# Kernel optimization log

Hardware: AMD Instinct MI355X
Metric: run time of the kernel (lower is better)

Reference implementation:

```python
import jax, jax.numpy as jnp
import numpy as np

# ---- problem sizes (would come from edge_index / init args in the torch module) ----
N = 10000      # number of nodes
E = 100000     # number of edges
C = 6          # channels per node
L = 6          # layers
B = 16         # batch
N_IN = 100     # input nodes  (nodes [0, N_IN))
N_OUT = 100    # output nodes (nodes [N-N_OUT, N))
EPS = 1e-5


def setup_inputs() -> dict:
    rng = np.random.default_rng(0)
    src = rng.integers(0, N, size=E).astype(np.int32)
    dst = rng.integers(0, N, size=E).astype(np.int32)

    input_mask = np.zeros(N, bool); input_mask[:N_IN] = True
    output_mask = np.zeros(N, bool); output_mask[N - N_OUT:] = True
    func_mask = ~(input_mask | output_mask)
    func_nodes = np.nonzero(func_mask)[0].astype(np.int32)
    F = func_nodes.size
    ii = np.arange(C, dtype=np.int32)

    # W1 (E -> C*N): edge e feeds all C channels of its dst node. nnz = E*C
    w1_rows = np.repeat(np.arange(E, dtype=np.int32), C)
    w1_cols = (dst[:, None] * C + ii[None, :]).reshape(-1)

    # W2 (C*N -> C*N): dense CxC block per function node. nnz = F*C*C
    base = np.repeat(func_nodes * C, C * C)
    w2_rows = base + np.tile(np.repeat(ii, C), F)
    w2_cols = base + np.tile(np.tile(ii, C), F)

    # W3 (C*N -> E): edge e reads the C channels of src(e) if src is a function node
    e_sel = np.nonzero(func_mask[src])[0].astype(np.int32)
    w3_rows = (src[e_sel][:, None] * C + ii[None, :]).reshape(-1)
    w3_cols = np.repeat(e_sel, C)

    # values: kaiming-style init with fan d (d=C for W1/W2, d=1 for W3)
    w1_vals = (rng.standard_normal(w1_rows.size) / np.sqrt(C)).astype(np.float32)
    w2_vals = (rng.standard_normal(w2_rows.size) / np.sqrt(C)).astype(np.float32)
    w3_vals = (rng.standard_normal(w3_rows.size) * 1.0).astype(np.float32)

    key = jax.random.key(0)
    x = jax.random.normal(key, (B, N), dtype=jnp.float32)

    return {
        "x": x,
        "src": jnp.asarray(src), "dst": jnp.asarray(dst),
        "output_mask": jnp.asarray(output_mask),
        "w1_rows": jnp.asarray(w1_rows), "w1_cols": jnp.asarray(w1_cols),
        "w1_vals": jnp.asarray(w1_vals), "b1": jnp.zeros((C * N,), jnp.float32),
        "w2_rows": jnp.asarray(w2_rows), "w2_cols": jnp.asarray(w2_cols),
        "w2_vals": jnp.asarray(w2_vals), "b2": jnp.zeros((C * N,), jnp.float32),
        "w3_rows": jnp.asarray(w3_rows), "w3_cols": jnp.asarray(w3_cols),
        "w3_vals": jnp.asarray(w3_vals), "b3": jnp.zeros((E,), jnp.float32),
        "gamma": jnp.ones((L,), jnp.float32), "beta": jnp.zeros((L,), jnp.float32),
    }


def _sp_lin(h, rows, cols, vals, bias, out_dim):
    # out[b, c] = sum_{k: cols[k]==c} h[b, rows[k]] * vals[k] + bias[c]
    contrib = h[:, rows] * vals  # [B, nnz]
    out = jnp.zeros((h.shape[0], out_dim), h.dtype).at[:, cols].add(contrib)
    return out + bias


def _batchnorm_scalar(z, g, b):
    # BatchNorm1d(1) on z.view(-1,1): single channel over all B*E elements (training mode)
    m = jnp.mean(z)
    v = jnp.mean(jnp.square(z - m))
    return (z - m) * jax.lax.rsqrt(v + EPS) * g + b


def reference(x, src, dst, output_mask,
              w1_rows, w1_cols, w1_vals, b1,
              w2_rows, w2_cols, w2_vals, b2,
              w3_rows, w3_cols, w3_vals, b3,
              gamma, beta):
    x0 = x[:, src]          # node2edge: [B, E]
    h = x0
    h_last = x0             # residual=True path
    for l in range(L):
        z = _sp_lin(h, w1_rows, w1_cols, w1_vals, b1, C * N)
        z = jax.nn.elu(z)
        z = _sp_lin(z, w2_rows, w2_cols, w2_vals, b2, C * N)
        z = jax.nn.elu(z)
        z = _sp_lin(z, w3_rows, w3_cols, w3_vals, b3, E)
        z = _batchnorm_scalar(z, gamma[l], beta[l])
        h = z + h_last
        h_last = h
    h = h / L
    # edge2node: scatter edge values to dst nodes, keep only output nodes
    node = jnp.zeros((x.shape[0], N), x.dtype).at[:, dst].add(h)
    return jnp.where(output_mask[None, :], node, 0.0)
```

## Files before the change

kernel.cpp:

```cpp
#include <hip/hip_runtime.h>
#include <math.h>

#define NN 10000
#define NE 100000
#define CC 6
#define LL 6
#define BB 16
#define FUNC_LO 100
#define FUNC_HI 9900
#define NOUT 100
#define EPSF 1e-5f
#define NSLOT 64

struct Slot { double s1, s2; double pad[6]; };

struct Params {
  const float *x, *w1v, *b1, *w2v, *b2, *w3v, *b3, *gamma, *beta;
  const int *src, *dst, *w3r, *w3c;
  float *out;
  int *row_start, *counts, *fill, *slot;
  int *row2, *counts2, *fill2, *csr2;
  uint4 *grec;
  uint4 *srec;
  unsigned short *sb3;
  float *xT, *h;
  unsigned short *z3a, *z3b;
  unsigned short *A;
  float *Cw;
  Slot *part, *baseS;
  int F, Ksel;
};

__device__ __forceinline__ float eluf(float x){ return x > 0.0f ? x : expm1f(x); }
__device__ __forceinline__ float bf2f(unsigned short h){
  union { unsigned int u; float f; } c; c.u = ((unsigned int)h)<<16; return c.f;
}
__device__ __forceinline__ unsigned short f2bf(float f){
  union { float f; unsigned int u; } c; c.f = f;
  return (unsigned short)((c.u + 0x7FFFu + ((c.u>>16)&1u)) >> 16);
}
__device__ __forceinline__ unsigned int packbf(float a, float b){
  return (unsigned int)f2bf(a) | ((unsigned int)f2bf(b)<<16);
}
__device__ __forceinline__ float2 ubf2(unsigned int u){
  union { unsigned int u; float f; } lo, hi;
  lo.u = u<<16; hi.u = u & 0xFFFF0000u;
  return make_float2(lo.f, hi.f);
}

__device__ void block_add_slot(double a, double q, Slot* sl){
  __shared__ double sb1[4], sb2[4];
  #pragma unroll
  for(int off=32;off;off>>=1){ a+=__shfl_down(a,off); q+=__shfl_down(q,off); }
  int wid = threadIdx.x>>6;
  if((threadIdx.x&63)==0){ sb1[wid]=a; sb2[wid]=q; }
  __syncthreads();
  if(threadIdx.x==0){
    double A=sb1[0]+sb1[1]+sb1[2]+sb1[3];
    double Q=sb2[0]+sb2[1]+sb2[2]+sb2[3];
    if(A!=0.0) atomicAdd(&sl->s1,A);
    if(Q!=0.0) atomicAdd(&sl->s2,Q);
  }
  __syncthreads();
}

__device__ void bn_params(const Slot* part, const Slot* baseS, float* m, float* inv){
  __shared__ double s_mv[2];
  if(threadIdx.x < NSLOT){
    double a = part[threadIdx.x].s1 + baseS[threadIdx.x].s1;
    double q = part[threadIdx.x].s2 + baseS[threadIdx.x].s2;
    #pragma unroll
    for(int off=32;off;off>>=1){ a+=__shfl_down(a,off); q+=__shfl_down(q,off); }
    if(threadIdx.x==0){
      const double cnt = (double)NE*(double)BB;
      double md = a/cnt, vd = q/cnt - md*md;
      s_mv[0]=md; s_mv[1]=1.0/sqrt(vd+(double)EPSF);
    }
  }
  __syncthreads();
  *m=(float)s_mv[0]; *inv=(float)s_mv[1];
  __syncthreads();
}

__global__ __launch_bounds__(256) void kw_P1(Params p){
  int tid = blockIdx.x*256 + threadIdx.x, nt = gridDim.x*256;
  for(int i=tid;i<NN*BB;i+=nt){ int n=i>>4, b=i&15; p.xT[i]=p.x[b*NN+n]; }
  for(int i=tid;i<BB*NN;i+=nt) p.out[i]=0.f;
  double a=0.0,q=0.0;
  for(int e=tid;e<NE;e+=nt){
    atomicAdd(&p.counts[p.dst[e]],1);
    int s=p.src[e];
    if(!(s>=FUNC_LO && s<FUNC_HI)){ double v=(double)p.b3[e]; a+=v; q+=v*v; }
  }
  for(int k=tid;k<p.Ksel;k+=nt){
    int s=p.w3r[k*CC]/CC;
    atomicAdd(&p.counts2[s-FUNC_LO],1);
  }
  block_add_slot(a*BB, q*BB, &p.baseS[blockIdx.x&(NSLOT-1)]);
}

__global__ __launch_bounds__(256) void kw_scan(Params p){
  __shared__ int s_scan[256];
  const int*  cin  = (blockIdx.x==0)? p.counts : p.counts2;
  int*        rout = (blockIdx.x==0)? p.row_start : p.row2;
  const int   nel  = (blockIdx.x==0)? NN : p.F;
  const int   CH   = (nel+255)/256;
  int t=threadIdx.x, base=t*CH, s=0;
  for(int k=0;k<CH;k++){ int i=base+k; if(i<nel) s+=cin[i]; }
  s_scan[t]=s; __syncthreads();
  for(int off=1;off<256;off<<=1){
    int v=(t>=off)?s_scan[t-off]:0; __syncthreads();
    s_scan[t]+=v; __syncthreads();
  }
  int run=s_scan[t]-s;
  for(int k=0;k<CH;k++){ int i=base+k; if(i<nel){ rout[i]=run; run+=cin[i]; } }
  if(t==255) rout[nel]=s_scan[255];
}

__global__ __launch_bounds__(256) void kw_fill(Params p){
  int tid = blockIdx.x*256 + threadIdx.x, nt = gridDim.x*256;
  for(int e=tid;e<NE;e+=nt){
    int n=p.dst[e];
    int pos=p.row_start[n]+atomicAdd(&p.fill[n],1);
    p.slot[e]=pos;
    const float* w=&p.w1v[e*CC];
    int s=p.src[e];
    float b3v=p.b3[e];
    p.grec[pos]=make_uint4(packbf(w[0],w[1]),packbf(w[2],w[3]),
                           packbf(w[4],w[5]),(unsigned int)s);
    if(!(s>=FUNC_LO && s<FUNC_HI)){
      unsigned int hb = f2bf(b3v);
      unsigned int pk = hb | (hb<<16);
      uint4 v4 = make_uint4(pk,pk,pk,pk);
      uint4* za=(uint4*)&p.z3a[pos*BB];
      uint4* zb=(uint4*)&p.z3b[pos*BB];
      za[0]=v4; za[1]=v4; zb[0]=v4; zb[1]=v4;
    }
  }
  for(int k=tid;k<p.Ksel;k+=nt){
    int fi=p.w3r[k*CC]/CC - FUNC_LO;
    int pos=p.row2[fi]+atomicAdd(&p.fill2[fi],1);
    p.csr2[pos]=k;
  }
}

template<int MODE>
__global__ __launch_bounds__(256) void kw_AB(Params p, int l,
    const unsigned short* __restrict__ z3p, unsigned short* __restrict__ z3c){
  int tid = blockIdx.x*256 + (int)threadIdx.x, nt = gridDim.x*256;
  float c1=0.f, c2=0.f;
  if(MODE>0){
    float m, inv;
    bn_params(p.part+(l-1)*NSLOT, p.baseS, &m, &inv);
    float g=p.gamma[l-1], be=p.beta[l-1];
    c1 = inv*g; c2 = be - m*c1;
  }
  const int FB2 = p.F*32;
  double a=0.0, q=0.0;
  for(int t=tid;t<FB2;t+=nt){
    int fi = t>>5;
    int u  = t&31, b = u&15, half = u>>4;
    int n  = FUNC_LO+fi;
    float acc[CC], cacc[CC];
    #pragma unroll
    for(int i=0;i<CC;i++){ acc[i]=0.f; cacc[i]=0.f; }
    int beg=p.row_start[n], end=p.row_start[n+1];
    int pp = beg + half;
    for(; pp+2<end; pp+=4){
      uint4 g0=p.grec[pp], g1=p.grec[pp+2];
      float2 wa0=ubf2(g0.x), wb0=ubf2(g0.y), wc0=ubf2(g0.z);
      float2 wa1=ubf2(g1.x), wb1=ubf2(g1.y), wc1=ubf2(g1.z);
      float hv0, hv1;
      if(MODE==0){
        int s0=(int)g0.w, s1=(int)g1.w;
        hv0 = p.xT[s0*BB+b];
        hv1 = p.xT[s1*BB+b];
        cacc[0]+=wa0.x+wa1.x; cacc[1]+=wa0.y+wa1.y; cacc[2]+=wb0.x+wb1.x;
        cacc[3]+=wb0.y+wb1.y; cacc[4]+=wc0.x+wc1.x; cacc[5]+=wc0.y+wc1.y;
      } else {
        hv0 = bf2f(z3p[pp*BB+b]);
        hv1 = bf2f(z3p[(pp+2)*BB+b]);
      }
      acc[0]+=hv0*wa0.x+hv1*wa1.x; acc[1]+=hv0*wa0.y+hv1*wa1.y;
      acc[2]+=hv0*wb0.x+hv1*wb1.x; acc[3]+=hv0*wb0.y+hv1*wb1.y;
      acc[4]+=hv0*wc0.x+hv1*wc1.x; acc[5]+=hv0*wc0.y+hv1*wc1.y;
    }
    if(pp<end){
      uint4 g0=p.grec[pp];
      float2 wa0=ubf2(g0.x), wb0=ubf2(g0.y), wc0=ubf2(g0.z);
      float hv0;
      if(MODE==0){
        int s0=(int)g0.w;
        hv0 = p.xT[s0*BB+b];
        cacc[0]+=wa0.x; cacc[1]+=wa0.y; cacc[2]+=wb0.x;
        cacc[3]+=wb0.y; cacc[4]+=wc0.x; cacc[5]+=wc0.y;
      } else {
        hv0 = bf2f(z3p[pp*BB+b]);
      }
      acc[0]+=hv0*wa0.x; acc[1]+=hv0*wa0.y; acc[2]+=hv0*wb0.x;
      acc[3]+=hv0*wb0.y; acc[4]+=hv0*wc0.x; acc[5]+=hv0*wc0.y;
    }
    float z1v[CC];
    #pragma unroll
    for(int i=0;i<CC;i++){
      acc[i] += __shfl_xor(acc[i],16);
      if(MODE==0){
        cacc[i] += __shfl_xor(cacc[i],16);
        if(half==0){
          p.A[(fi*CC+i)*BB+b] = f2bf(acc[i]);
          if(b==0) p.Cw[fi*CC+i] = cacc[i];
        }
        z1v[i] = eluf(acc[i] + p.b1[n*CC+i]);
      } else {
        float Aold = bf2f(p.A[(fi*CC+i)*BB+b]);
        float Cv   = p.Cw[fi*CC+i];
        float Anew = Aold + c1*acc[i] + c2*Cv;
        if(half==0) p.A[(fi*CC+i)*BB+b] = f2bf(Anew);
        z1v[i] = eluf(Anew + p.b1[n*CC+i]);
      }
    }
    const float* W2=&p.w2v[fi*36];
    float z2[CC];
    #pragma unroll
    for(int jj=0;jj<CC;jj++){
      float o=p.b2[n*CC+jj];
      #pragma unroll
      for(int i=0;i<CC;i++) o+=z1v[i]*W2[i*CC+jj];
      z2[jj]=eluf(o);
    }
    int bg2=p.row2[fi], en2=p.row2[fi+1];
    if(MODE==0){
      for(int sp=bg2+half;sp<en2;sp+=2){
        int k=p.csr2[sp];
        int e=p.w3c[k*CC];
        const float* w=&p.w3v[k*CC];
        float b3v=p.b3[e];
        int sl=p.slot[e];
        float2 a01=ubf2(packbf(w[0],w[1]));
        float2 a23=ubf2(packbf(w[2],w[3]));
        float2 a45=ubf2(packbf(w[4],w[5]));
        if(b==0){
          p.srec[sp]=make_uint4(packbf(w[0],w[1]),packbf(w[2],w[3]),
                                packbf(w[4],w[5]),(unsigned int)sl);
          p.sb3[sp]=f2bf(b3v);
        }
        float o = b3v + z2[0]*a01.x+z2[1]*a01.y+z2[2]*a23.x
                      + z2[3]*a23.y+z2[4]*a45.x+z2[5]*a45.y;
        z3c[sl*BB+b]=f2bf(o);
        a+=o; q+=(double)o*o;
      }
    } else {
      for(int sp=bg2+half;sp<en2;sp+=2){
        uint4 s4=p.srec[sp];
        float b3v=bf2f(p.sb3[sp]);
        float2 a01=ubf2(s4.x), a23=ubf2(s4.y), a45=ubf2(s4.z);
        float o = b3v + z2[0]*a01.x + z2[1]*a01.y + z2[2]*a23.x
                      + z2[3]*a23.y + z2[4]*a45.x + z2[5]*a45.y;
        int sl=(int)s4.w;
        z3c[sl*BB+b]=f2bf(o);
        a+=o; q+=(double)o*o;
      }
    }
  }
  if(MODE>0){
    int outBeg = p.row_start[FUNC_HI];
    int tot = (p.row_start[NN]-outBeg)*BB;
    for(int u=tid; u<tot; u+=nt){
      int pp=outBeg+(u>>4); int bb=u&15;
      float zb=bf2f(z3p[pp*BB+bb]);
      float hb;
      if(MODE==1){
        uint4 g=p.grec[pp];
        int s=(int)g.w;
        hb=p.xT[s*BB+bb];
      } else {
        hb=p.h[pp*BB+bb];
      }
      p.h[pp*BB+bb]=hb+zb*c1+c2;
    }
  }
  block_add_slot(a,q,&p.part[l*NSLOT+(blockIdx.x&(NSLOT-1))]);
}

__global__ __launch_bounds__(256) void kw_out(Params p, const unsigned short* __restrict__ z3p){
  int tid = blockIdx.x*256 + threadIdx.x, nt = gridDim.x*256;
  float m,inv;
  bn_params(p.part+(LL-1)*NSLOT, p.baseS, &m, &inv);
  float g=p.gamma[LL-1], be=p.beta[LL-1];
  float c1=inv*g, c2=be-m*c1;
  for(int t=tid;t<NOUT*BB;t+=nt){
    int j=t>>4, b=t&15;
    int n=FUNC_HI+j;
    float acc=0.f;
    int beg=p.row_start[n], end=p.row_start[n+1];
    for(int pp=beg;pp<end;++pp){
      acc += p.h[pp*BB+b] + bf2f(z3p[pp*BB+b])*c1 + c2;
    }
    p.out[b*NN+n]=acc*(1.0f/(float)LL);
  }
}

extern "C" void kernel_launch(void* const* d_in, const int* in_sizes, int n_in,
                              void* d_out, int out_size, void* d_ws, size_t ws_size,
                              hipStream_t stream){
  Params p;
  p.x    =(const float*)d_in[0];
  p.src  =(const int*)  d_in[1];
  p.dst  =(const int*)  d_in[2];
  p.w1v  =(const float*)d_in[6];
  p.b1   =(const float*)d_in[7];
  p.w2v  =(const float*)d_in[10];
  p.b2   =(const float*)d_in[11];
  p.w3r  =(const int*)  d_in[12];
  p.w3c  =(const int*)  d_in[13];
  p.w3v  =(const float*)d_in[14];
  p.b3   =(const float*)d_in[15];
  p.gamma=(const float*)d_in[16];
  p.beta =(const float*)d_in[17];
  p.out  =(float*)d_out;
  p.F    = in_sizes[8]/36;
  p.Ksel = in_sizes[12]/CC;

  char* ws=(char*)d_ws; size_t off=0;
  auto alloc=[&](size_t bytes)->char*{
    char* q=ws+off; off=(off+bytes+255)&~(size_t)255; return q;
  };
  p.row_start=(int*)  alloc((NN+1)*sizeof(int));
  p.row2     =(int*)  alloc((size_t)(p.F+1)*sizeof(int));
  p.slot     =(int*)  alloc(NE*sizeof(int));
  p.csr2     =(int*)  alloc(NE*sizeof(int));
  p.grec     =(uint4*)alloc((size_t)NE*sizeof(uint4));
  p.srec     =(uint4*)alloc((size_t)NE*sizeof(uint4));
  p.sb3      =(unsigned short*)alloc((size_t)NE*sizeof(unsigned short));
  p.xT       =(float*)alloc((size_t)NN*BB*sizeof(float));
  p.h        =(float*)alloc((size_t)NE*BB*sizeof(float));
  p.z3a      =(unsigned short*)alloc((size_t)NE*BB*sizeof(unsigned short));
  p.z3b      =(unsigned short*)alloc((size_t)NE*BB*sizeof(unsigned short));
  p.A        =(unsigned short*)alloc((size_t)p.F*CC*BB*sizeof(unsigned short));
  p.Cw       =(float*)alloc((size_t)p.F*CC*sizeof(float));
  p.counts   =(int*)  alloc(NN*sizeof(int));
  p.fill     =(int*)  alloc(NN*sizeof(int));
  p.counts2  =(int*)  alloc((size_t)p.F*sizeof(int));
  p.fill2    =(int*)  alloc((size_t)p.F*sizeof(int));
  p.part     =(Slot*) alloc((size_t)LL*NSLOT*sizeof(Slot));
  p.baseS    =(Slot*) alloc((size_t)NSLOT*sizeof(Slot));
  (void)ws_size; (void)n_in; (void)out_size;

  size_t zspan = (char*)(p.baseS+NSLOT) - (char*)p.counts;
  hipMemsetAsync(p.counts, 0, zspan, stream);

  unsigned short* bufs[2] = { p.z3a, p.z3b };
  const int gridAB = (p.F*32 + 255)/256;

  kw_P1  <<<512,256,0,stream>>>(p);
  kw_scan<<<2,  256,0,stream>>>(p);
  kw_fill<<<512,256,0,stream>>>(p);
  kw_AB<0><<<gridAB,256,0,stream>>>(p, 0, bufs[1], bufs[0]);
  kw_AB<1><<<gridAB,256,0,stream>>>(p, 1, bufs[0], bufs[1]);
  for(int l=2;l<LL;l++){
    kw_AB<2><<<gridAB,256,0,stream>>>(p, l, bufs[(l^1)&1], bufs[l&1]);
  }
  kw_out<<<(NOUT*BB+255)/256,256,0,stream>>>(p, bufs[(LL-1)&1]);
}
```

Before: 159.9 us.

## Fold scan into P1 and compute BN stats once via last-block finalize

The separate scan kernel is removed: the last block to finish kw_P1, detected with an atomic done counter, performs both prefix scans. Each kw_AB block now counts itself in on finish, and the last block reduces the batchnorm partial slots and writes mean and inverse std to a small global array. Later kernels read those two floats instead of every block re-reducing 64 slots. This saves one launch and redundant per-block reductions, at the cost of a serial tail where a single block does the scan work, plus extra atomics and fences.

After: 366.1 us. 2.29x slower.

```diff
diff --git a/kernel.cpp b/kernel.cpp
--- a/kernel.cpp
+++ b/kernel.cpp
@@ -28,6 +28,8 @@
   unsigned short *A;
   float *Cw;
   Slot *part, *baseS;
+  float2 *mv;
+  int *done;
   int F, Ksel;
 };
 
@@ -64,22 +66,44 @@
   __syncthreads();
 }
 
-__device__ void bn_params(const Slot* part, const Slot* baseS, float* m, float* inv){
-  __shared__ double s_mv[2];
-  if(threadIdx.x < NSLOT){
-    double a = part[threadIdx.x].s1 + baseS[threadIdx.x].s1;
-    double q = part[threadIdx.x].s2 + baseS[threadIdx.x].s2;
+__device__ void finalize_bn(const Params& p, int l){
+  __shared__ int sFin;
+  if(threadIdx.x==0){
+    __threadfence();
+    int old=atomicAdd(&p.done[l],1);
+    sFin = (old==(int)gridDim.x-1);
+  }
+  __syncthreads();
+  if(sFin && threadIdx.x<64){
+    Slot* pl=&p.part[l*NSLOT+threadIdx.x];
+    double s1=atomicAdd(&pl->s1,0.0)+p.baseS[threadIdx.x].s1;
+    double s2=atomicAdd(&pl->s2,0.0)+p.baseS[threadIdx.x].s2;
     #pragma unroll
-    for(int off=32;off;off>>=1){ a+=__shfl_down(a,off); q+=__shfl_down(q,off); }
+    for(int off=32;off;off>>=1){ s1+=__shfl_down(s1,off); s2+=__shfl_down(s2,off); }
     if(threadIdx.x==0){
-      const double cnt = (double)NE*(double)BB;
-      double md = a/cnt, vd = q/cnt - md*md;
-      s_mv[0]=md; s_mv[1]=1.0/sqrt(vd+(double)EPSF);
-    }
-  }
-  __syncthreads();
-  *m=(float)s_mv[0]; *inv=(float)s_mv[1];
-  __syncthreads();
+      const double cnt=(double)NE*(double)BB;
+      double md=s1/cnt, vd=s2/cnt-md*md;
+      p.mv[l]=make_float2((float)md,(float)(1.0/sqrt(vd+(double)EPSF)));
+    }
+  }
+}
+
+__device__ void scan_one(int* cin, int* rout, int nel){
+  __shared__ int s_scan[256];
+  const int CH=(nel+255)/256;
+  int t=threadIdx.x, base=t*CH, s=0;
+  for(int k=0;k<CH;k++){ int i=base+k; if(i<nel) s+=atomicAdd(&cin[i],0); }
+  s_scan[t]=s; __syncthreads();
+  for(int off=1;off<256;off<<=1){
+    int v=(t>=off)?s_scan[t-off]:0; __syncthreads();
+    s_scan[t]+=v; __syncthreads();
+  }
+  int run=s_scan[t]-s;
+  for(int k=0;k<CH;k++){
+    int i=base+k;
+    if(i<nel){ rout[i]=run; run+=atomicAdd(&cin[i],0); }
+  }
+  if(t==255) rout[nel]=s_scan[255];
 }
 
 __global__ __launch_bounds__(256) void kw_P1(Params p){
@@ -97,24 +121,17 @@
     atomicAdd(&p.counts2[s-FUNC_LO],1);
   }
   block_add_slot(a*BB, q*BB, &p.baseS[blockIdx.x&(NSLOT-1)]);
-}
-
-__global__ __launch_bounds__(256) void kw_scan(Params p){
-  __shared__ int s_scan[256];
-  const int*  cin  = (blockIdx.x==0)? p.counts : p.counts2;
-  int*        rout = (blockIdx.x==0)? p.row_start : p.row2;
-  const int   nel  = (blockIdx.x==0)? NN : p.F;
-  const int   CH   = (nel+255)/256;
-  int t=threadIdx.x, base=t*CH, s=0;
-  for(int k=0;k<CH;k++){ int i=base+k; if(i<nel) s+=cin[i]; }
-  s_scan[t]=s; __syncthreads();
-  for(int off=1;off<256;off<<=1){
-    int v=(t>=off)?s_scan[t-off]:0; __syncthreads();
-    s_scan[t]+=v; __syncthreads();
-  }
-  int run=s_scan[t]-s;
-  for(int k=0;k<CH;k++){ int i=base+k; if(i<nel){ rout[i]=run; run+=cin[i]; } }
-  if(t==255) rout[nel]=s_scan[255];
+  __shared__ int sFin;
+  if(threadIdx.x==0){
+    __threadfence();
+    int old=atomicAdd(&p.done[LL],1);
+    sFin=(old==(int)gridDim.x-1);
+  }
+  __syncthreads();
+  if(!sFin) return;
+  scan_one(p.counts, p.row_start, NN);
+  __syncthreads();
+  scan_one(p.counts2, p.row2, p.F);
 }
 
 __global__ __launch_bounds__(256) void kw_fill(Params p){
@@ -150,10 +167,9 @@
   int tid = blockIdx.x*256 + (int)threadIdx.x, nt = gridDim.x*256;
   float c1=0.f, c2=0.f;
   if(MODE>0){
-    float m, inv;
-    bn_params(p.part+(l-1)*NSLOT, p.baseS, &m, &inv);
+    float2 mi = p.mv[l-1];
     float g=p.gamma[l-1], be=p.beta[l-1];
-    c1 = inv*g; c2 = be - m*c1;
+    c1 = mi.y*g; c2 = be - mi.x*c1;
   }
   const int FB2 = p.F*32;
   double a=0.0, q=0.0;
@@ -280,14 +296,14 @@
     }
   }
   block_add_slot(a,q,&p.part[l*NSLOT+(blockIdx.x&(NSLOT-1))]);
+  finalize_bn(p,l);
 }
 
 __global__ __launch_bounds__(256) void kw_out(Params p, const unsigned short* __restrict__ z3p){
   int tid = blockIdx.x*256 + threadIdx.x, nt = gridDim.x*256;
-  float m,inv;
-  bn_params(p.part+(LL-1)*NSLOT, p.baseS, &m, &inv);
+  float2 mi = p.mv[LL-1];
   float g=p.gamma[LL-1], be=p.beta[LL-1];
-  float c1=inv*g, c2=be-m*c1;
+  float c1=mi.y*g, c2=be-mi.x*c1;
   for(int t=tid;t<NOUT*BB;t+=nt){
     int j=t>>4, b=t&15;
     int n=FUNC_HI+j;
@@ -338,22 +354,23 @@
   p.z3b      =(unsigned short*)alloc((size_t)NE*BB*sizeof(unsigned short));
   p.A        =(unsigned short*)alloc((size_t)p.F*CC*BB*sizeof(unsigned short));
   p.Cw       =(float*)alloc((size_t)p.F*CC*sizeof(float));
+  p.mv       =(float2*)alloc(LL*sizeof(float2));
   p.counts   =(int*)  alloc(NN*sizeof(int));
   p.fill     =(int*)  alloc(NN*sizeof(int));
   p.counts2  =(int*)  alloc((size_t)p.F*sizeof(int));
   p.fill2    =(int*)  alloc((size_t)p.F*sizeof(int));
   p.part     =(Slot*) alloc((size_t)LL*NSLOT*sizeof(Slot));
   p.baseS    =(Slot*) alloc((size_t)NSLOT*sizeof(Slot));
+  p.done     =(int*)  alloc(8*sizeof(int));
   (void)ws_size; (void)n_in; (void)out_size;
 
-  size_t zspan = (char*)(p.baseS+NSLOT) - (char*)p.counts;
+  size_t zspan = (char*)(p.done+8) - (char*)p.counts;
   hipMemsetAsync(p.counts, 0, zspan, stream);
 
   unsigned short* bufs[2] = { p.z3a, p.z3b };
   const int gridAB = (p.F*32 + 255)/256;
 
   kw_P1  <<<512,256,0,stream>>>(p);
-  kw_scan<<<2,  256,0,stream>>>(p);
   kw_fill<<<512,256,0,stream>>>(p);
   kw_AB<0><<<gridAB,256,0,stream>>>(p, 0, bufs[1], bufs[0]);
   kw_AB<1><<<gridAB,256,0,stream>>>(p, 1, bufs[0], bufs[1]);
```
